# Kernel optimization log

Measured on AMD Instinct MI355X. Metric: run time of the kernel, lower is better.

## Reference

```python
import jax, jax.numpy as jnp
import numpy as np
import math

NUM_REG_TOKENS = 0  # encoder.num_register_tokens
EPS = 1e-12         # matches torch F.normalize eps


def _l2norm(x):
    # F.normalize(x, dim=-1): x / max(||x||, eps)
    n = jnp.sqrt(jnp.sum(x * x, axis=-1, keepdims=True))
    return x / jnp.maximum(n, EPS)


def setup_inputs() -> dict:
    key = jax.random.key(0)
    k1, k2 = jax.random.split(key)
    L, N, S, T, D = 3, 8, 4, 1370, 768  # 3 interested layers, T = 1 + 37^2 patches
    q_feats = jax.random.normal(k1, (L, N, T, D), dtype=jnp.float32)
    s_feats = jax.random.normal(k2, (L, N * S, T, D), dtype=jnp.float32)
    return {"q_feats": q_feats, "s_feats": s_feats}


def reference(q_feats, s_feats):
    # fuse_feature: mean over stacked interested layers
    xq = jnp.mean(q_feats, axis=0)   # [N, T, D]
    xs = jnp.mean(s_feats, axis=0)   # [N*S, T, D]
    N = xq.shape[0]
    Q = xq.shape[1] - 1 - NUM_REG_TOKENS
    side = int(math.isqrt(Q))
    # drop class (+register) tokens
    xq = xq[:, 1 + NUM_REG_TOKENS:, :]                 # [N, Q, D]
    xs = xs[:, 1 + NUM_REG_TOKENS:, :]                 # [N*S, Q, D]
    xs = xs.reshape(N, -1, xs.shape[-1])               # [N, S*Q, D]
    xq = _l2norm(xq)
    xs = _l2norm(xs)
    # cosine distance + 1-NN min over support tokens
    sim = jnp.einsum('nqd,nsd->nqs', xq, xs)           # [N, Q, S*Q]
    dist = jnp.min(1.0 - sim, axis=-1)                 # [N, Q]
    return dist.reshape(N, 1, side, side)
```

## Files before the change

kernel.cpp:

```cpp
#include <hip/hip_runtime.h>
#include <hip/hip_bf16.h>

typedef __attribute__((ext_vector_type(4))) float f32x4;
typedef __attribute__((ext_vector_type(8))) int i32x8;

#define T_TOK 1370
#define DDIM  768
#define SCV   1369
#define SCP   1408
#define MQP   1536
#define NB    8
#define NSLAB 32
#define NST   22
#define NMT   6

#define MEMFENCE asm volatile("" ::: "memory")
#define BARRIER  do { __builtin_amdgcn_s_barrier(); MEMFENCE; } while (0)
#define VMCNT0   asm volatile("s_waitcnt vmcnt(0)" ::: "memory")

#define GLOAD_LDS16(g, l)                                                     \
  __builtin_amdgcn_global_load_lds(                                           \
      (const __attribute__((address_space(1))) unsigned int*)(g),             \
      (__attribute__((address_space(3))) unsigned int*)(l), 16, 0, 0)

extern "C" __global__ __launch_bounds__(192) void prep_kernel(
    const float* __restrict__ src, unsigned char* __restrict__ dst,
    size_t lstride)
{
  const int row  = blockIdx.x;
  const int slab = blockIdx.y;
  const int t    = threadIdx.x;
  unsigned char* drow = dst + ((size_t)slab * gridDim.x + row) * DDIM;
  if (row >= SCV) {
    reinterpret_cast<unsigned int*>(drow)[t] = 0u;
    return;
  }
  const float* base = src + ((size_t)slab * T_TOK + row + 1) * DDIM;
  float4 a = reinterpret_cast<const float4*>(base)[t];
  float4 b = reinterpret_cast<const float4*>(base + lstride)[t];
  float4 c = reinterpret_cast<const float4*>(base + 2 * lstride)[t];
  const float k3 = 1.0f / 3.0f;
  float4 m;
  m.x = (a.x + b.x + c.x) * k3;
  m.y = (a.y + b.y + c.y) * k3;
  m.z = (a.z + b.z + c.z) * k3;
  m.w = (a.w + b.w + c.w) * k3;
  float ss = m.x * m.x + m.y * m.y + m.z * m.z + m.w * m.w;
  #pragma unroll
  for (int d = 1; d < 64; d <<= 1) ss += __shfl_xor(ss, d);
  __shared__ float wsum[3];
  if ((t & 63) == 0) wsum[t >> 6] = ss;
  __syncthreads();
  float tot = wsum[0] + wsum[1] + wsum[2];
  float rn = 1.0f / fmaxf(sqrtf(tot), 1e-12f);
  int pk = __builtin_amdgcn_cvt_pk_fp8_f32(m.x * rn, m.y * rn, 0, false);
  pk = __builtin_amdgcn_cvt_pk_fp8_f32(m.z * rn, m.w * rn, pk, true);
  reinterpret_cast<unsigned int*>(drow)[t] = (unsigned int)pk;
}

extern "C" __global__ __launch_bounds__(512, 2) void simmax_kernel(
    const unsigned char* __restrict__ xq,
    const unsigned char* __restrict__ xs,
    float* __restrict__ part)
{
  const int flat = blockIdx.x;
  const int swz  = (flat & 7) * (NMT * NST) + (flat >> 3);
  const int n    = swz / (NMT * NST);
  const int idx  = swz - n * (NMT * NST);
  const int mt   = idx % NMT;
  const int st   = idx / NMT;

  const int tid  = threadIdx.x;
  const int lane = tid & 63;
  const int w    = tid >> 6;
  const int wr   = w >> 2;
  const int wcn  = w & 3;
  const int l15  = lane & 15, l4 = lane >> 4;

  __shared__ unsigned char ring[2][65536];
  __shared__ float sfold[1024];

  const unsigned char* gA = xq + ((size_t)n * MQP + (size_t)mt * 256) * DDIM;
  const unsigned char* gB = xs + ((size_t)n * 4 * SCP + (size_t)st * 256) * DDIM;

  int goff[4], ldso[4];
  #pragma unroll
  for (int i = 0; i < 4; ++i) {
    int c = w * 4 + i;
    int r = c * 8 + (lane >> 3);
    goff[i] = r * DDIM + (((lane & 7) ^ (r & 7)) << 4);
    ldso[i] = c * 1024;
  }

  int aoff[8], boff[4];
  #pragma unroll
  for (int mf = 0; mf < 8; ++mf) {
    int row = wr * 128 + mf * 16 + l15;
    aoff[mf] = row * 128 + ((((l4 << 1) ^ (row & 7))) << 4);
  }
  #pragma unroll
  for (int nf = 0; nf < 4; ++nf) {
    int row = wcn * 64 + nf * 16 + l15;
    boff[nf] = 32768 + row * 128 + ((((l4 << 1) ^ (row & 7))) << 4);
  }

  f32x4 acc[8][4];
  {
    f32x4 zz = {0.f, 0.f, 0.f, 0.f};
    #pragma unroll
    for (int a = 0; a < 8; ++a)
      #pragma unroll
      for (int b = 0; b < 4; ++b) acc[a][b] = zz;
  }

  #define ISSUE(KT, RB)                                                      \
    do {                                                                     \
      const unsigned char* ga_ = gA + (KT) * 128;                            \
      const unsigned char* gb_ = gB + (KT) * 128;                            \
      unsigned char* la_ = ring[RB];                                         \
      unsigned char* lb_ = ring[RB] + 32768;                                 \
      _Pragma("unroll") for (int i = 0; i < 4; ++i)                          \
        GLOAD_LDS16(ga_ + goff[i], la_ + ldso[i]);                           \
      _Pragma("unroll") for (int i = 0; i < 4; ++i)                          \
        GLOAD_LDS16(gb_ + goff[i], lb_ + ldso[i]);                           \
    } while (0)

  ISSUE(0, 0);
  VMCNT0;
  BARRIER;

  for (int kt = 0; kt < 6; ++kt) {
    if (kt + 1 < 6) ISSUE(kt + 1, (kt + 1) & 1);

    const char* Cb = reinterpret_cast<const char*>(ring[kt & 1]);
    i32x8 bfr[4];
    #pragma unroll
    for (int nf = 0; nf < 4; ++nf) {
      int4 lo = *reinterpret_cast<const int4*>(Cb + boff[nf]);
      int4 hi = *reinterpret_cast<const int4*>(Cb + (boff[nf] ^ 16));
      bfr[nf] = i32x8{lo.x, lo.y, lo.z, lo.w, hi.x, hi.y, hi.z, hi.w};
    }
    __builtin_amdgcn_s_setprio(1);
    #pragma unroll
    for (int mf = 0; mf < 8; ++mf) {
      int4 lo = *reinterpret_cast<const int4*>(Cb + aoff[mf]);
      int4 hi = *reinterpret_cast<const int4*>(Cb + (aoff[mf] ^ 16));
      i32x8 af = i32x8{lo.x, lo.y, lo.z, lo.w, hi.x, hi.y, hi.z, hi.w};
      #pragma unroll
      for (int nf = 0; nf < 4; ++nf)
        acc[mf][nf] = __builtin_amdgcn_mfma_scale_f32_16x16x128_f8f6f4(
            af, bfr[nf], acc[mf][nf], 0, 0, 0, 127, 0, 127);
    }
    __builtin_amdgcn_s_setprio(0);

    if (kt + 1 < 6) VMCNT0;
    if (kt < 5) BARRIER;
  }

  bool colv[4];
  #pragma unroll
  for (int nf = 0; nf < 4; ++nf) {
    int col = st * 256 + wcn * 64 + nf * 16 + l15;
    int within = col - (col / SCP) * SCP;
    colv[nf] = within < SCV;
  }

  float rm[8][4];
  #pragma unroll
  for (int mf = 0; mf < 8; ++mf)
    #pragma unroll
    for (int j = 0; j < 4; ++j) {
      float v = -1e30f;
      #pragma unroll
      for (int nf = 0; nf < 4; ++nf)
        if (colv[nf]) v = fmaxf(v, acc[mf][nf][j]);
      rm[mf][j] = v;
    }

  #pragma unroll
  for (int msk = 1; msk < 16; msk <<= 1)
    #pragma unroll
    for (int mf = 0; mf < 8; ++mf)
      #pragma unroll
      for (int j = 0; j < 4; ++j)
        rm[mf][j] = fmaxf(rm[mf][j], __shfl_xor(rm[mf][j], msk));

  __syncthreads();
  if (l15 == 0) {
    #pragma unroll
    for (int mf = 0; mf < 8; ++mf)
      #pragma unroll
      for (int j = 0; j < 4; ++j) {
        int r = wr * 128 + mf * 16 + l4 * 4 + j;
        sfold[wcn * 256 + r] = rm[mf][j];
      }
  }
  __syncthreads();
  if (tid < 256) {
    float v = fmaxf(fmaxf(sfold[tid], sfold[256 + tid]),
                    fmaxf(sfold[512 + tid], sfold[768 + tid]));
    part[((size_t)n * NST + st) * MQP + (size_t)mt * 256 + tid] = v;
  }
}

extern "C" __global__ void finalize_kernel(const float* __restrict__ part,
                                           float* __restrict__ out) {
  int i = blockIdx.x * 256 + threadIdx.x;
  if (i >= NB * SCV) return;
  int n = i / SCV, q = i - n * SCV;
  const float* p = part + (size_t)n * NST * MQP + q;
  float m = p[0];
  #pragma unroll 4
  for (int g = 1; g < NST; ++g) m = fmaxf(m, p[(size_t)g * MQP]);
  out[i] = 1.0f - m;
}

extern "C" void kernel_launch(void* const* d_in, const int* in_sizes, int n_in,
                              void* d_out, int out_size, void* d_ws, size_t ws_size,
                              hipStream_t stream) {
  const float* q_feats = (const float*)d_in[0];
  const float* s_feats = (const float*)d_in[1];
  float* out = (float*)d_out;

  char* ws = (char*)d_ws;
  const size_t xq_bytes = (size_t)NB * MQP * DDIM;
  const size_t xs_bytes = (size_t)NSLAB * SCP * DDIM;
  unsigned char* xq = (unsigned char*)ws;
  unsigned char* xs = (unsigned char*)(ws + xq_bytes);
  float* part       = (float*)(ws + xq_bytes + xs_bytes);

  prep_kernel<<<dim3(MQP, NB), 192, 0, stream>>>(
      q_feats, xq, (size_t)NB * T_TOK * DDIM);
  prep_kernel<<<dim3(SCP, NSLAB), 192, 0, stream>>>(
      s_feats, xs, (size_t)NSLAB * T_TOK * DDIM);
  simmax_kernel<<<dim3(NB * NMT * NST), 512, 0, stream>>>(xq, xs, part);
  finalize_kernel<<<dim3((NB * SCV + 255) / 256), 256, 0, stream>>>(part, out);
}
```

Before: 182.0 us.

## Load A fragments directly from global memory, stage only B in LDS

The query (A) operand is no longer staged through LDS. Each wave now reads its MFMA A fragments straight from global memory, and only the support (B) tile is double-buffered in LDS, which halves the LDS footprint and the async copy traffic per k-step. The explicit vmcnt waits and raw barriers are replaced by __syncthreads. The cost is that global-load latency now sits directly ahead of the MFMAs. Each A row is also fetched by four waves (the four wcn groups), which raises L2 traffic and relies on cache hits.

```diff
diff --git a/kernel.cpp b/kernel.cpp
--- a/kernel.cpp
+++ b/kernel.cpp
@@ -15,8 +15,6 @@
 #define NMT   6
 
 #define MEMFENCE asm volatile("" ::: "memory")
-#define BARRIER  do { __builtin_amdgcn_s_barrier(); MEMFENCE; } while (0)
-#define VMCNT0   asm volatile("s_waitcnt vmcnt(0)" ::: "memory")
 
 #define GLOAD_LDS16(g, l)                                                     \
   __builtin_amdgcn_global_load_lds(                                           \
@@ -77,7 +75,7 @@
   const int wcn  = w & 3;
   const int l15  = lane & 15, l4 = lane >> 4;
 
-  __shared__ unsigned char ring[2][65536];
+  __shared__ unsigned char bbuf[2][32768];
   __shared__ float sfold[1024];
 
   const unsigned char* gA = xq + ((size_t)n * MQP + (size_t)mt * 256) * DDIM;
@@ -92,16 +90,16 @@
     ldso[i] = c * 1024;
   }
 
-  int aoff[8], boff[4];
-  #pragma unroll
-  for (int mf = 0; mf < 8; ++mf) {
-    int row = wr * 128 + mf * 16 + l15;
-    aoff[mf] = row * 128 + ((((l4 << 1) ^ (row & 7))) << 4);
-  }
+  int aoffg[8];
+  #pragma unroll
+  for (int mf = 0; mf < 8; ++mf)
+    aoffg[mf] = (wr * 128 + mf * 16 + l15) * DDIM + l4 * 32;
+
+  int boff[4];
   #pragma unroll
   for (int nf = 0; nf < 4; ++nf) {
     int row = wcn * 64 + nf * 16 + l15;
-    boff[nf] = 32768 + row * 128 + ((((l4 << 1) ^ (row & 7))) << 4);
+    boff[nf] = row * 128 + ((((l4 << 1) ^ (row & 7))) << 4);
   }
 
   f32x4 acc[8][4];
@@ -113,26 +111,21 @@
       for (int b = 0; b < 4; ++b) acc[a][b] = zz;
   }
 
-  #define ISSUE(KT, RB)                                                      \
+  #define ISSUE_B(KT, RB)                                                    \
     do {                                                                     \
-      const unsigned char* ga_ = gA + (KT) * 128;                            \
       const unsigned char* gb_ = gB + (KT) * 128;                            \
-      unsigned char* la_ = ring[RB];                                         \
-      unsigned char* lb_ = ring[RB] + 32768;                                 \
-      _Pragma("unroll") for (int i = 0; i < 4; ++i)                          \
-        GLOAD_LDS16(ga_ + goff[i], la_ + ldso[i]);                           \
+      unsigned char* lb_ = bbuf[RB];                                         \
       _Pragma("unroll") for (int i = 0; i < 4; ++i)                          \
         GLOAD_LDS16(gb_ + goff[i], lb_ + ldso[i]);                           \
     } while (0)
 
-  ISSUE(0, 0);
-  VMCNT0;
-  BARRIER;
+  ISSUE_B(0, 0);
+  __syncthreads();
 
   for (int kt = 0; kt < 6; ++kt) {
-    if (kt + 1 < 6) ISSUE(kt + 1, (kt + 1) & 1);
-
-    const char* Cb = reinterpret_cast<const char*>(ring[kt & 1]);
+    if (kt + 1 < 6) ISSUE_B(kt + 1, (kt + 1) & 1);
+
+    const char* Cb = reinterpret_cast<const char*>(bbuf[kt & 1]);
     i32x8 bfr[4];
     #pragma unroll
     for (int nf = 0; nf < 4; ++nf) {
@@ -140,11 +133,13 @@
       int4 hi = *reinterpret_cast<const int4*>(Cb + (boff[nf] ^ 16));
       bfr[nf] = i32x8{lo.x, lo.y, lo.z, lo.w, hi.x, hi.y, hi.z, hi.w};
     }
+
+    const unsigned char* ga = gA + kt * 128;
     __builtin_amdgcn_s_setprio(1);
     #pragma unroll
     for (int mf = 0; mf < 8; ++mf) {
-      int4 lo = *reinterpret_cast<const int4*>(Cb + aoff[mf]);
-      int4 hi = *reinterpret_cast<const int4*>(Cb + (aoff[mf] ^ 16));
+      int4 lo = *reinterpret_cast<const int4*>(ga + aoffg[mf]);
+      int4 hi = *reinterpret_cast<const int4*>(ga + aoffg[mf] + 16);
       i32x8 af = i32x8{lo.x, lo.y, lo.z, lo.w, hi.x, hi.y, hi.z, hi.w};
       #pragma unroll
       for (int nf = 0; nf < 4; ++nf)
@@ -153,8 +148,7 @@
     }
     __builtin_amdgcn_s_setprio(0);
 
-    if (kt + 1 < 6) VMCNT0;
-    if (kt < 5) BARRIER;
+    __syncthreads();
   }
 
   bool colv[4];
```

After: 255.7 us. +40.5%, slower.

## Deepen B prefetch to triple buffer and interleave LDS reads with MFMA phases

Applied to the files above, without the earlier changes.

Splits the shared ring into a double-buffered A tile and a triple-buffered B tile, so B loads are issued two k-steps ahead. It waits on partial vmcnt instead of draining all loads. Each k-step is broken into four phases that read two A fragments, sync, then run MFMAs, so LDS reads interleave with matrix work. This adds many more barriers per iteration and raises LDS use from about 132KB to 160KB, which may limit occupancy to one block per CU despite launch bounds of 2.

```diff
diff --git a/kernel.cpp b/kernel.cpp
--- a/kernel.cpp
+++ b/kernel.cpp
@@ -16,7 +16,7 @@
 
 #define MEMFENCE asm volatile("" ::: "memory")
 #define BARRIER  do { __builtin_amdgcn_s_barrier(); MEMFENCE; } while (0)
-#define VMCNT0   asm volatile("s_waitcnt vmcnt(0)" ::: "memory")
+#define LGKM0    asm volatile("s_waitcnt lgkmcnt(0)" ::: "memory")
 
 #define GLOAD_LDS16(g, l)                                                     \
   __builtin_amdgcn_global_load_lds(                                           \
@@ -77,8 +77,8 @@
   const int wcn  = w & 3;
   const int l15  = lane & 15, l4 = lane >> 4;
 
-  __shared__ unsigned char ring[2][65536];
-  __shared__ float sfold[1024];
+  __shared__ unsigned char Abuf[2][32768];
+  __shared__ unsigned char Bbuf[3][32768];
 
   const unsigned char* gA = xq + ((size_t)n * MQP + (size_t)mt * 256) * DDIM;
   const unsigned char* gB = xs + ((size_t)n * 4 * SCP + (size_t)st * 256) * DDIM;
@@ -101,7 +101,7 @@
   #pragma unroll
   for (int nf = 0; nf < 4; ++nf) {
     int row = wcn * 64 + nf * 16 + l15;
-    boff[nf] = 32768 + row * 128 + ((((l4 << 1) ^ (row & 7))) << 4);
+    boff[nf] = row * 128 + ((((l4 << 1) ^ (row & 7))) << 4);
   }
 
   f32x4 acc[8][4];
@@ -113,48 +113,79 @@
       for (int b = 0; b < 4; ++b) acc[a][b] = zz;
   }
 
-  #define ISSUE(KT, RB)                                                      \
+  #define ISSUE_A(KT)                                                        \
     do {                                                                     \
       const unsigned char* ga_ = gA + (KT) * 128;                            \
-      const unsigned char* gb_ = gB + (KT) * 128;                            \
-      unsigned char* la_ = ring[RB];                                         \
-      unsigned char* lb_ = ring[RB] + 32768;                                 \
+      unsigned char* la_ = Abuf[(KT) & 1];                                   \
       _Pragma("unroll") for (int i = 0; i < 4; ++i)                          \
         GLOAD_LDS16(ga_ + goff[i], la_ + ldso[i]);                           \
+    } while (0)
+  #define ISSUE_B(KT)                                                        \
+    do {                                                                     \
+      const unsigned char* gb_ = gB + (KT) * 128;                            \
+      unsigned char* lb_ = Bbuf[(KT) % 3];                                   \
       _Pragma("unroll") for (int i = 0; i < 4; ++i)                          \
         GLOAD_LDS16(gb_ + goff[i], lb_ + ldso[i]);                           \
     } while (0)
 
-  ISSUE(0, 0);
-  VMCNT0;
+  #define READ_FRAG(PTR, OFF, DST)                                           \
+    do {                                                                     \
+      int4 lo_ = *reinterpret_cast<const int4*>((PTR) + (OFF));              \
+      int4 hi_ = *reinterpret_cast<const int4*>((PTR) + ((OFF) ^ 16));       \
+      DST = i32x8{lo_.x, lo_.y, lo_.z, lo_.w, hi_.x, hi_.y, hi_.z, hi_.w};   \
+    } while (0)
+
+  ISSUE_A(0);
+  ISSUE_B(0);
+  ISSUE_B(1);
+  asm volatile("s_waitcnt vmcnt(4)" ::: "memory");
   BARRIER;
 
   for (int kt = 0; kt < 6; ++kt) {
-    if (kt + 1 < 6) ISSUE(kt + 1, (kt + 1) & 1);
-
-    const char* Cb = reinterpret_cast<const char*>(ring[kt & 1]);
-    i32x8 bfr[4];
+    if (kt < 5) ISSUE_A(kt + 1);
+    if (kt < 4) ISSUE_B(kt + 2);
+
+    const char* Ab = reinterpret_cast<const char*>(Abuf[kt & 1]);
+    const char* Bb = reinterpret_cast<const char*>(Bbuf[kt % 3]);
+
+    i32x8 bfr[4], af0, af1;
+    #pragma unroll
+    for (int nf = 0; nf < 4; ++nf) READ_FRAG(Bb, boff[nf], bfr[nf]);
+    READ_FRAG(Ab, aoff[0], af0);
+    READ_FRAG(Ab, aoff[1], af1);
+    BARRIER; LGKM0;
+    __builtin_amdgcn_s_setprio(1);
     #pragma unroll
     for (int nf = 0; nf < 4; ++nf) {
-      int4 lo = *reinterpret_cast<const int4*>(Cb + boff[nf]);
-      int4 hi = *reinterpret_cast<const int4*>(Cb + (boff[nf] ^ 16));
-      bfr[nf] = i32x8{lo.x, lo.y, lo.z, lo.w, hi.x, hi.y, hi.z, hi.w};
-    }
-    __builtin_amdgcn_s_setprio(1);
-    #pragma unroll
-    for (int mf = 0; mf < 8; ++mf) {
-      int4 lo = *reinterpret_cast<const int4*>(Cb + aoff[mf]);
-      int4 hi = *reinterpret_cast<const int4*>(Cb + (aoff[mf] ^ 16));
-      i32x8 af = i32x8{lo.x, lo.y, lo.z, lo.w, hi.x, hi.y, hi.z, hi.w};
-      #pragma unroll
-      for (int nf = 0; nf < 4; ++nf)
-        acc[mf][nf] = __builtin_amdgcn_mfma_scale_f32_16x16x128_f8f6f4(
-            af, bfr[nf], acc[mf][nf], 0, 0, 0, 127, 0, 127);
+      acc[0][nf] = __builtin_amdgcn_mfma_scale_f32_16x16x128_f8f6f4(
+          af0, bfr[nf], acc[0][nf], 0, 0, 0, 127, 0, 127);
+      acc[1][nf] = __builtin_amdgcn_mfma_scale_f32_16x16x128_f8f6f4(
+          af1, bfr[nf], acc[1][nf], 0, 0, 0, 127, 0, 127);
     }
     __builtin_amdgcn_s_setprio(0);
-
-    if (kt + 1 < 6) VMCNT0;
-    if (kt < 5) BARRIER;
+    BARRIER;
+
+    #pragma unroll
+    for (int p = 1; p < 4; ++p) {
+      i32x8 afa, afb;
+      READ_FRAG(Ab, aoff[2 * p], afa);
+      READ_FRAG(Ab, aoff[2 * p + 1], afb);
+      if (p == 3) {
+        if (kt < 4)       asm volatile("s_waitcnt vmcnt(4)" ::: "memory");
+        else if (kt == 4) asm volatile("s_waitcnt vmcnt(0)" ::: "memory");
+      }
+      BARRIER; LGKM0;
+      __builtin_amdgcn_s_setprio(1);
+      #pragma unroll
+      for (int nf = 0; nf < 4; ++nf) {
+        acc[2 * p][nf] = __builtin_amdgcn_mfma_scale_f32_16x16x128_f8f6f4(
+            afa, bfr[nf], acc[2 * p][nf], 0, 0, 0, 127, 0, 127);
+        acc[2 * p + 1][nf] = __builtin_amdgcn_mfma_scale_f32_16x16x128_f8f6f4(
+            afb, bfr[nf], acc[2 * p + 1][nf], 0, 0, 0, 127, 0, 127);
+      }
+      __builtin_amdgcn_s_setprio(0);
+      BARRIER;
+    }
   }
 
   bool colv[4];
@@ -186,6 +217,7 @@
         rm[mf][j] = fmaxf(rm[mf][j], __shfl_xor(rm[mf][j], msk));
 
   __syncthreads();
+  float* sfold = reinterpret_cast<float*>(&Abuf[0][0]);
   if (l15 == 0) {
     #pragma unroll
     for (int mf = 0; mf < 8; ++mf)
```

After: 193.0 us. 6.1% more time.
